# Performance work log

Measured on AMD Instinct MI355X. Metric: run time of the kernel, lower is better.

## Reference

```python
import jax, jax.numpy as jnp
import numpy as np

HIDDEN_DIM = 4096
NUM_EXPERTS = 64
THRESHOLD = 0.8


def setup_inputs() -> dict:
    key = jax.random.key(0)
    kx, kw = jax.random.split(key)
    x = jax.random.normal(kx, (4, 4096, HIDDEN_DIM), dtype=jnp.float32)
    # gate weight init: normal(0, 0.1), bias zeros (as in nn.init calls)
    W = jax.random.normal(kw, (HIDDEN_DIM, NUM_EXPERTS), dtype=jnp.float32) * 0.1
    b = jnp.zeros((NUM_EXPERTS,), dtype=jnp.float32)
    return {"x": x, "W": W, "b": b}


def reference(x, W, b):
    # logits: [B, S, E]
    logits = jnp.einsum('bsh,he->bse', x, W) + b
    probs = jax.nn.softmax(logits, axis=-1)
    # descending sort over experts
    order = jnp.argsort(-probs, axis=-1)                        # [B,S,E] int
    sorted_probs = jnp.take_along_axis(probs, order, axis=-1)   # [B,S,E]
    cum = jnp.cumsum(sorted_probs, axis=-1)
    mask = cum >= THRESHOLD                                     # [B,S,E] bool
    k_values = jnp.argmax(mask.astype(jnp.float32), axis=-1) + 1
    never = ~jnp.any(mask, axis=-1)
    k_values = jnp.where(never, NUM_EXPERTS, k_values)          # [B,S] int
    # Vectorized mask-and-scatter replacing the per-token Python loop.
    # Padded to NUM_EXPERTS (static max_k) for jit compatibility; slots
    # beyond k get expert=-1, prob=0 exactly as the torch fill defaults.
    slot = jnp.arange(NUM_EXPERTS)                              # [E]
    sel = slot[None, None, :] < k_values[..., None]             # [B,S,E]
    selected_experts = jnp.where(sel, order, -1)
    selected_probs = jnp.where(sel, sorted_probs, 0.0)
    return selected_experts, selected_probs, k_values
```

## Files before the change

kernel.cpp:

```cpp
#include <hip/hip_runtime.h>
#include <math.h>

#define HID 4096
#define NEXP 64
#define NTOK 16384
#define PSTR 65

typedef __attribute__((ext_vector_type(8))) short short8;
typedef __attribute__((ext_vector_type(8))) __bf16 bf16x8;
typedef __attribute__((ext_vector_type(4))) float f32x4;

__global__ __launch_bounds__(256) void wfrag_kernel(
    const float* __restrict__ W, short* __restrict__ wfh,
    short* __restrict__ wfl, unsigned int* __restrict__ flag_count) {
  if (blockIdx.x == 0 && threadIdx.x == 0) *flag_count = 0u;
  int gid = blockIdx.x * 256 + threadIdx.x;
  int l  = gid & 63;
  int nt = (gid >> 6) & 3;
  int ks = gid >> 8;
  int e  = nt * 16 + (l & 15);
  int k0 = ks * 32 + (l >> 4) * 8;
  bf16x8 h8, l8;
#pragma unroll
  for (int j = 0; j < 8; ++j) {
    float w = W[(size_t)(k0 + j) * NEXP + e];
    __bf16 h = (__bf16)w;
    h8[j] = h;
    l8[j] = (__bf16)(w - (float)h);
  }
  ((short8*)wfh)[gid] = __builtin_bit_cast(short8, h8);
  ((short8*)wfl)[gid] = __builtin_bit_cast(short8, l8);
}

template <int P>
__device__ __forceinline__ void issue_b(const short8* wh, const short8* wl,
                                        short8 (&rbh)[2][4],
                                        short8 (&rbl)[2][4], int cc) {
#pragma unroll
  for (int nt = 0; nt < 4; ++nt) {
    rbh[P][nt] = wh[cc * 256 + nt * 64];
    rbl[P][nt] = wl[cc * 256 + nt * 64];
  }
}

template <int P>
__device__ __forceinline__ void issue_g(const float* const (&xp)[4][2],
                                        float* wavebase, int cc) {
#pragma unroll
  for (int st = 0; st < 4; ++st)
#pragma unroll
    for (int p = 0; p < 2; ++p)
      __builtin_amdgcn_global_load_lds(xp[st][p] + cc * 32,
                                       wavebase + P * 2048 + st * 512 + p * 256,
                                       16, 0, 0);
}

template <int P>
__device__ __forceinline__ void compute_c(const float* wavebase,
                                          short8 (&rbh)[2][4],
                                          short8 (&rbl)[2][4],
                                          f32x4 (&acc)[4][4], int l) {
  const int lr = l >> 4;
  const int s0 = ((2 * lr) ^ (l & 7)) * 16;
  const char* cb = (const char*)(wavebase + P * 2048);
#pragma unroll
  for (int st = 0; st < 4; ++st) {
    const char* rowbase =
        cb + st * 2048 + ((l >> 3) & 1) * 1024 + (l & 7) * 128;
    float4 lo = *(const float4*)(rowbase + s0);
    float4 hi = *(const float4*)(rowbase + (s0 ^ 16));
    float xv[8] = {lo.x, lo.y, lo.z, lo.w, hi.x, hi.y, hi.z, hi.w};
    bf16x8 ah, al;
#pragma unroll
    for (int j = 0; j < 8; ++j) {
      __bf16 h = (__bf16)xv[j];
      ah[j] = h;
      al[j] = (__bf16)(xv[j] - (float)h);
    }
#pragma unroll
    for (int nt = 0; nt < 4; ++nt) {
      bf16x8 vh = __builtin_bit_cast(bf16x8, rbh[P][nt]);
      bf16x8 vl = __builtin_bit_cast(bf16x8, rbl[P][nt]);
      acc[st][nt] = __builtin_amdgcn_mfma_f32_16x16x32_bf16(ah, vh, acc[st][nt], 0, 0, 0);
      acc[st][nt] = __builtin_amdgcn_mfma_f32_16x16x32_bf16(al, vh, acc[st][nt], 0, 0, 0);
      acc[st][nt] = __builtin_amdgcn_mfma_f32_16x16x32_bf16(ah, vl, acc[st][nt], 0, 0, 0);
      acc[st][nt] = __builtin_amdgcn_mfma_f32_16x16x32_bf16(al, vl, acc[st][nt], 0, 0, 0);
    }
  }
}

#define SB __builtin_amdgcn_sched_barrier(0)
#define WAIT16 asm volatile("s_waitcnt vmcnt(16)" ::: "memory")
#define WAIT0  asm volatile("s_waitcnt vmcnt(0)" ::: "memory")

__global__ __launch_bounds__(512, 2) void gemm_route_kernel(
    const float* __restrict__ x, const short* __restrict__ wfh,
    const short* __restrict__ wfl, const float* __restrict__ b,
    float* __restrict__ out_exp, float* __restrict__ out_prob,
    float* __restrict__ out_k, unsigned int* __restrict__ flag_count,
    int* __restrict__ flag_list) {
  __shared__ float smem[8 * 64 * PSTR];

  const int t = threadIdx.x;
  const int w = t >> 6;
  const int l = t & 63;
  const int lr = l >> 4;
  const int m0 = blockIdx.x * 64;
  const int kq = w * (HID / 8);
  const int start = (blockIdx.x >> 3) & 15;

  float* wavebase = smem + w * 4096;

  const float* xp[4][2];
#pragma unroll
  for (int st = 0; st < 4; ++st)
#pragma unroll
    for (int p = 0; p < 2; ++p) {
      int g = (l & 7) ^ (l >> 3);
      int row = m0 + st * 16 + 8 * p + (l >> 3);
      xp[st][p] = x + (size_t)row * HID + kq + g * 4;
    }

  const short8* wh = (const short8*)wfh + (size_t)(w * 16) * 256 + l;
  const short8* wl = (const short8*)wfl + (size_t)(w * 16) * 256 + l;

  f32x4 acc[4][4];
#pragma unroll
  for (int st = 0; st < 4; ++st)
#pragma unroll
    for (int nt = 0; nt < 4; ++nt) acc[st][nt] = (f32x4){0.f, 0.f, 0.f, 0.f};

  short8 rbh[2][4], rbl[2][4];

  issue_b<0>(wh, wl, rbh, rbl, start);
  SB;
  issue_g<0>(xp, wavebase, start);
  SB;

#pragma unroll 1
  for (int c2 = 0; c2 < 7; ++c2) {
    const int i0 = 2 * c2;
    issue_b<1>(wh, wl, rbh, rbl, (start + i0 + 1) & 15);
    SB;
    issue_g<1>(xp, wavebase, (start + i0 + 1) & 15);
    SB;
    WAIT16;
    SB;
    compute_c<0>(wavebase, rbh, rbl, acc, l);

    issue_b<0>(wh, wl, rbh, rbl, (start + i0 + 2) & 15);
    SB;
    issue_g<0>(xp, wavebase, (start + i0 + 2) & 15);
    SB;
    WAIT16;
    SB;
    compute_c<1>(wavebase, rbh, rbl, acc, l);
  }
  issue_b<1>(wh, wl, rbh, rbl, (start + 15) & 15);
  SB;
  issue_g<1>(xp, wavebase, (start + 15) & 15);
  SB;
  WAIT16;
  SB;
  compute_c<0>(wavebase, rbh, rbl, acc, l);
  WAIT0;
  SB;
  compute_c<1>(wavebase, rbh, rbl, acc, l);

  __syncthreads();
  float* part = smem;
#pragma unroll
  for (int st = 0; st < 4; ++st)
#pragma unroll
    for (int nt = 0; nt < 4; ++nt)
#pragma unroll
      for (int r = 0; r < 4; ++r)
        part[(w * 64 + st * 16 + lr * 4 + r) * PSTR + nt * 16 + (l & 15)] =
            acc[st][nt][r];
  __syncthreads();

  const float bias = b[l];
  for (int it = 0; it < 8; ++it) {
    const int tl = w * 8 + it;
    float a0 = part[(0 * 64 + tl) * PSTR + l];
    float a1 = part[(1 * 64 + tl) * PSTR + l];
    float a2 = part[(2 * 64 + tl) * PSTR + l];
    float a3 = part[(3 * 64 + tl) * PSTR + l];
    float a4 = part[(4 * 64 + tl) * PSTR + l];
    float a5 = part[(5 * 64 + tl) * PSTR + l];
    float a6 = part[(6 * 64 + tl) * PSTR + l];
    float a7 = part[(7 * 64 + tl) * PSTR + l];
    float lgv = ((a0 + a1) + (a2 + a3)) + ((a4 + a5) + (a6 + a7)) + bias;

    float mx = lgv;
#pragma unroll
    for (int off = 32; off; off >>= 1) mx = fmaxf(mx, __shfl_xor(mx, off));
    float ev = expf(lgv - mx);
    float sm = ev;
#pragma unroll
    for (int off = 32; off; off >>= 1) sm += __shfl_xor(sm, off);
    float pr = ev / sm;

    float sp = pr;
    int   si = l;
#pragma unroll
    for (int k = 2; k <= 64; k <<= 1) {
#pragma unroll
      for (int j = k >> 1; j > 0; j >>= 1) {
        float op = __shfl_xor(sp, j);
        int   oi = __shfl_xor(si, j);
        bool cmp  = (sp > op) || (sp == op && si < oi);
        bool keep = (cmp == (((l & k) == 0) == ((l & j) == 0)));
        if (!keep) { sp = op; si = oi; }
      }
    }

    float c = sp;
#pragma unroll
    for (int off = 1; off < 64; off <<= 1) {
      float tp = __shfl_up(c, off);
      if (l >= off) c += tp;
    }

    unsigned long long m = __ballot(c >= 0.8f);
    int kv = (m == 0ULL) ? NEXP : __ffsll(m);

    float spn = __shfl_down(sp, 1);
    bool pairRisk = (l < kv) && (l < 63) && ((sp - spn) < 1e-3f * (sp + spn));
    bool cumRisk  = fabsf(c - 0.8f) < 3e-4f;
    bool flagged  = (__ballot(pairRisk || cumRisk) != 0ULL);

    bool sel = l < kv;
    const int tok = m0 + tl;
    size_t base = (size_t)tok * NEXP;
    out_exp[base + l]  = sel ? (float)si : -1.0f;
    out_prob[base + l] = sel ? sp : 0.0f;
    if (l == 0) {
      out_k[tok] = (float)kv;
      if (flagged) {
        unsigned int idx = atomicAdd(flag_count, 1u);
        flag_list[idx] = tok;
      }
    }
  }
}

__global__ __launch_bounds__(256) void router_repair(
    const float* __restrict__ x, const float* __restrict__ W,
    const float* __restrict__ b, const unsigned int* __restrict__ flag_count,
    const int* __restrict__ flag_list, float* __restrict__ out_exp,
    float* __restrict__ out_prob, float* __restrict__ out_k) {
  __shared__ double part[4][NEXP];
  const int t = threadIdx.x;
  const int e = t & 63;
  const int c = t >> 6;
  const int n = (int)*flag_count;

  for (int i = blockIdx.x; i < n; i += gridDim.x) {
    const int tok = flag_list[i];
    const float* xrow = x + (size_t)tok * HID;
    double s = 0.0;
    const int k0 = c * (HID / 4);
#pragma unroll 8
    for (int k = k0; k < k0 + HID / 4; ++k)
      s = fma((double)xrow[k], (double)W[(size_t)k * NEXP + e], s);
    part[c][e] = s;
    __syncthreads();

    if (t < 64) {
      double lgv = ((part[0][e] + part[1][e]) + part[2][e]) + part[3][e] +
                   (double)b[e];
      double mx = lgv;
#pragma unroll
      for (int off = 32; off; off >>= 1) mx = fmax(mx, __shfl_xor(mx, off));
      double ev = exp(lgv - mx);
      double sm = ev;
#pragma unroll
      for (int off = 32; off; off >>= 1) sm += __shfl_xor(sm, off);
      double p = ev / sm;

      double sp = p;
      int    si = e;
#pragma unroll
      for (int k = 2; k <= 64; k <<= 1) {
#pragma unroll
        for (int j = k >> 1; j > 0; j >>= 1) {
          double op = __shfl_xor(sp, j);
          int    oi = __shfl_xor(si, j);
          bool cmp  = (sp > op) || (sp == op && si < oi);
          bool keep = (cmp == (((e & k) == 0) == ((e & j) == 0)));
          if (!keep) { sp = op; si = oi; }
        }
      }

      double cc = sp;
#pragma unroll
      for (int off = 1; off < 64; off <<= 1) {
        double tp = __shfl_up(cc, off);
        if (e >= off) cc += tp;
      }

      unsigned long long m = __ballot(cc >= 0.8);
      int kv = (m == 0ULL) ? NEXP : __ffsll(m);

      bool sel = e < kv;
      size_t base = (size_t)tok * NEXP;
      out_exp[base + e]  = sel ? (float)si : -1.0f;
      out_prob[base + e] = sel ? (float)sp : 0.0f;
      if (e == 0) out_k[tok] = (float)kv;
    }
    __syncthreads();
  }
}

extern "C" void kernel_launch(void* const* d_in, const int* in_sizes, int n_in,
                              void* d_out, int out_size, void* d_ws,
                              size_t ws_size, hipStream_t stream) {
  const float* x = (const float*)d_in[0];
  const float* W = (const float*)d_in[1];
  const float* b = (const float*)d_in[2];

  float* out_exp  = (float*)d_out;
  float* out_prob = out_exp + (size_t)NTOK * NEXP;
  float* out_k    = out_prob + (size_t)NTOK * NEXP;

  short* wfh = (short*)d_ws;
  short* wfl = (short*)((char*)d_ws + (size_t)512 * 1024);
  unsigned int* flag_count = (unsigned int*)((char*)d_ws + (size_t)1024 * 1024);
  int* flag_list = (int*)((char*)d_ws + (size_t)1024 * 1024 + 256);

  wfrag_kernel<<<128, 256, 0, stream>>>(W, wfh, wfl, flag_count);
  gemm_route_kernel<<<NTOK / 64, 512, 0, stream>>>(
      x, wfh, wfl, b, out_exp, out_prob, out_k, flag_count, flag_list);
  router_repair<<<128, 256, 0, stream>>>(x, W, b, flag_count, flag_list,
                                         out_exp, out_prob, out_k);
}
```

Before: 118.2 us.

## Fuse fp64 repair into GEMM kernel and deepen weight-fragment prefetch pipeline

Drops the separate router_repair launch. Each GEMM block now collects its flagged tokens in shared memory and recomputes them in fp64 in-block after routing, removing the global atomic list and one kernel launch. The K loop is fully unrolled with compile-time chunk steps, and the weight-fragment register buffer goes from 2 to 4 stages so B loads are issued two chunks ahead. The old per-block rotated start chunk is removed. Risks are higher register pressure from the extra buffers, a tail on blocks that have flagged tokens, and loss of the staggering that spread the weight reads across blocks.

```diff
diff --git a/kernel.cpp b/kernel.cpp
--- a/kernel.cpp
+++ b/kernel.cpp
@@ -12,8 +12,7 @@
 
 __global__ __launch_bounds__(256) void wfrag_kernel(
     const float* __restrict__ W, short* __restrict__ wfh,
-    short* __restrict__ wfl, unsigned int* __restrict__ flag_count) {
-  if (blockIdx.x == 0 && threadIdx.x == 0) *flag_count = 0u;
+    short* __restrict__ wfl) {
   int gid = blockIdx.x * 256 + threadIdx.x;
   int l  = gid & 63;
   int nt = (gid >> 6) & 3;
@@ -32,14 +31,19 @@
   ((short8*)wfl)[gid] = __builtin_bit_cast(short8, l8);
 }
 
-template <int P>
+#define SB __builtin_amdgcn_sched_barrier(0)
+#define WAIT24 asm volatile("s_waitcnt vmcnt(24)" ::: "memory")
+#define WAIT16 asm volatile("s_waitcnt vmcnt(16)" ::: "memory")
+#define WAIT0  asm volatile("s_waitcnt vmcnt(0)" ::: "memory")
+
+template <int S>
 __device__ __forceinline__ void issue_b(const short8* wh, const short8* wl,
-                                        short8 (&rbh)[2][4],
-                                        short8 (&rbl)[2][4], int cc) {
+                                        short8 (&rbh)[4][4],
+                                        short8 (&rbl)[4][4], int cc) {
 #pragma unroll
   for (int nt = 0; nt < 4; ++nt) {
-    rbh[P][nt] = wh[cc * 256 + nt * 64];
-    rbl[P][nt] = wl[cc * 256 + nt * 64];
+    rbh[S][nt] = wh[cc * 256 + nt * 64];
+    rbl[S][nt] = wl[cc * 256 + nt * 64];
   }
 }
 
@@ -55,10 +59,10 @@
                                        16, 0, 0);
 }
 
-template <int P>
+template <int P, int S>
 __device__ __forceinline__ void compute_c(const float* wavebase,
-                                          short8 (&rbh)[2][4],
-                                          short8 (&rbl)[2][4],
+                                          short8 (&rbh)[4][4],
+                                          short8 (&rbl)[4][4],
                                           f32x4 (&acc)[4][4], int l) {
   const int lr = l >> 4;
   const int s0 = ((2 * lr) ^ (l & 7)) * 16;
@@ -79,8 +83,8 @@
     }
 #pragma unroll
     for (int nt = 0; nt < 4; ++nt) {
-      bf16x8 vh = __builtin_bit_cast(bf16x8, rbh[P][nt]);
-      bf16x8 vl = __builtin_bit_cast(bf16x8, rbl[P][nt]);
+      bf16x8 vh = __builtin_bit_cast(bf16x8, rbh[S][nt]);
+      bf16x8 vl = __builtin_bit_cast(bf16x8, rbl[S][nt]);
       acc[st][nt] = __builtin_amdgcn_mfma_f32_16x16x32_bf16(ah, vh, acc[st][nt], 0, 0, 0);
       acc[st][nt] = __builtin_amdgcn_mfma_f32_16x16x32_bf16(al, vh, acc[st][nt], 0, 0, 0);
       acc[st][nt] = __builtin_amdgcn_mfma_f32_16x16x32_bf16(ah, vl, acc[st][nt], 0, 0, 0);
@@ -89,17 +93,33 @@
   }
 }
 
-#define SB __builtin_amdgcn_sched_barrier(0)
-#define WAIT16 asm volatile("s_waitcnt vmcnt(16)" ::: "memory")
-#define WAIT0  asm volatile("s_waitcnt vmcnt(0)" ::: "memory")
+template <int N>
+__device__ __forceinline__ void chunk_step(const float* const (&xp)[4][2],
+                                           float* wavebase, const short8* wh,
+                                           const short8* wl,
+                                           short8 (&rbh)[4][4],
+                                           short8 (&rbl)[4][4],
+                                           f32x4 (&acc)[4][4], int l) {
+  if constexpr (N + 1 < 16) issue_g<(N + 1) & 1>(xp, wavebase, N + 1);
+  SB;
+  if constexpr (N + 2 < 16) issue_b<(N + 2) & 3>(wh, wl, rbh, rbl, N + 2);
+  SB;
+  if constexpr (N <= 13) { WAIT24; }
+  else if constexpr (N == 14) { WAIT16; }
+  else { WAIT0; }
+  SB;
+  compute_c<N & 1, N & 3>(wavebase, rbh, rbl, acc, l);
+  SB;
+}
 
 __global__ __launch_bounds__(512, 2) void gemm_route_kernel(
-    const float* __restrict__ x, const short* __restrict__ wfh,
-    const short* __restrict__ wfl, const float* __restrict__ b,
-    float* __restrict__ out_exp, float* __restrict__ out_prob,
-    float* __restrict__ out_k, unsigned int* __restrict__ flag_count,
-    int* __restrict__ flag_list) {
+    const float* __restrict__ x, const float* __restrict__ W,
+    const short* __restrict__ wfh, const short* __restrict__ wfl,
+    const float* __restrict__ b, float* __restrict__ out_exp,
+    float* __restrict__ out_prob, float* __restrict__ out_k) {
   __shared__ float smem[8 * 64 * PSTR];
+  __shared__ int s_cnt;
+  __shared__ int s_toks[64];
 
   const int t = threadIdx.x;
   const int w = t >> 6;
@@ -107,7 +127,8 @@
   const int lr = l >> 4;
   const int m0 = blockIdx.x * 64;
   const int kq = w * (HID / 8);
-  const int start = (blockIdx.x >> 3) & 15;
+
+  if (t == 0) s_cnt = 0;
 
   float* wavebase = smem + w * 4096;
 
@@ -130,42 +151,31 @@
 #pragma unroll
     for (int nt = 0; nt < 4; ++nt) acc[st][nt] = (f32x4){0.f, 0.f, 0.f, 0.f};
 
-  short8 rbh[2][4], rbl[2][4];
-
-  issue_b<0>(wh, wl, rbh, rbl, start);
-  SB;
-  issue_g<0>(xp, wavebase, start);
-  SB;
-
-#pragma unroll 1
-  for (int c2 = 0; c2 < 7; ++c2) {
-    const int i0 = 2 * c2;
-    issue_b<1>(wh, wl, rbh, rbl, (start + i0 + 1) & 15);
-    SB;
-    issue_g<1>(xp, wavebase, (start + i0 + 1) & 15);
-    SB;
-    WAIT16;
-    SB;
-    compute_c<0>(wavebase, rbh, rbl, acc, l);
-
-    issue_b<0>(wh, wl, rbh, rbl, (start + i0 + 2) & 15);
-    SB;
-    issue_g<0>(xp, wavebase, (start + i0 + 2) & 15);
-    SB;
-    WAIT16;
-    SB;
-    compute_c<1>(wavebase, rbh, rbl, acc, l);
-  }
-  issue_b<1>(wh, wl, rbh, rbl, (start + 15) & 15);
-  SB;
-  issue_g<1>(xp, wavebase, (start + 15) & 15);
-  SB;
-  WAIT16;
-  SB;
-  compute_c<0>(wavebase, rbh, rbl, acc, l);
-  WAIT0;
-  SB;
-  compute_c<1>(wavebase, rbh, rbl, acc, l);
+  short8 rbh[4][4], rbl[4][4];
+
+  issue_b<0>(wh, wl, rbh, rbl, 0);
+  SB;
+  issue_g<0>(xp, wavebase, 0);
+  SB;
+  issue_b<1>(wh, wl, rbh, rbl, 1);
+  SB;
+
+  chunk_step<0>(xp, wavebase, wh, wl, rbh, rbl, acc, l);
+  chunk_step<1>(xp, wavebase, wh, wl, rbh, rbl, acc, l);
+  chunk_step<2>(xp, wavebase, wh, wl, rbh, rbl, acc, l);
+  chunk_step<3>(xp, wavebase, wh, wl, rbh, rbl, acc, l);
+  chunk_step<4>(xp, wavebase, wh, wl, rbh, rbl, acc, l);
+  chunk_step<5>(xp, wavebase, wh, wl, rbh, rbl, acc, l);
+  chunk_step<6>(xp, wavebase, wh, wl, rbh, rbl, acc, l);
+  chunk_step<7>(xp, wavebase, wh, wl, rbh, rbl, acc, l);
+  chunk_step<8>(xp, wavebase, wh, wl, rbh, rbl, acc, l);
+  chunk_step<9>(xp, wavebase, wh, wl, rbh, rbl, acc, l);
+  chunk_step<10>(xp, wavebase, wh, wl, rbh, rbl, acc, l);
+  chunk_step<11>(xp, wavebase, wh, wl, rbh, rbl, acc, l);
+  chunk_step<12>(xp, wavebase, wh, wl, rbh, rbl, acc, l);
+  chunk_step<13>(xp, wavebase, wh, wl, rbh, rbl, acc, l);
+  chunk_step<14>(xp, wavebase, wh, wl, rbh, rbl, acc, l);
+  chunk_step<15>(xp, wavebase, wh, wl, rbh, rbl, acc, l);
 
   __syncthreads();
   float* part = smem;
@@ -238,38 +248,39 @@
     if (l == 0) {
       out_k[tok] = (float)kv;
       if (flagged) {
-        unsigned int idx = atomicAdd(flag_count, 1u);
-        flag_list[idx] = tok;
+        int idx = atomicAdd(&s_cnt, 1);
+        if (idx < 64) s_toks[idx] = tl;
       }
     }
   }
-}
-
-__global__ __launch_bounds__(256) void router_repair(
-    const float* __restrict__ x, const float* __restrict__ W,
-    const float* __restrict__ b, const unsigned int* __restrict__ flag_count,
-    const int* __restrict__ flag_list, float* __restrict__ out_exp,
-    float* __restrict__ out_prob, float* __restrict__ out_k) {
-  __shared__ double part[4][NEXP];
-  const int t = threadIdx.x;
-  const int e = t & 63;
-  const int c = t >> 6;
-  const int n = (int)*flag_count;
-
-  for (int i = blockIdx.x; i < n; i += gridDim.x) {
-    const int tok = flag_list[i];
-    const float* xrow = x + (size_t)tok * HID;
-    double s = 0.0;
-    const int k0 = c * (HID / 4);
+
+  __syncthreads();
+  int cnt = s_cnt;
+  if (cnt > 64) cnt = 64;
+  double* dpart = (double*)smem;
+  const int g = w >> 2;
+  const int q = w & 3;
+
+  for (int i = 0; i < cnt; i += 2) {
+    const int which = i + g;
+    const bool active = which < cnt;
+    int tok = 0;
+    if (active) {
+      tok = m0 + s_toks[which];
+      const float* xr = x + (size_t)tok * HID;
+      double s = 0.0;
+      const int k0 = q * (HID / 4);
 #pragma unroll 8
-    for (int k = k0; k < k0 + HID / 4; ++k)
-      s = fma((double)xrow[k], (double)W[(size_t)k * NEXP + e], s);
-    part[c][e] = s;
+      for (int k = k0; k < k0 + HID / 4; ++k)
+        s = fma((double)xr[k], (double)W[(size_t)k * NEXP + l], s);
+      dpart[(g * 4 + q) * 64 + l] = s;
+    }
     __syncthreads();
-
-    if (t < 64) {
-      double lgv = ((part[0][e] + part[1][e]) + part[2][e]) + part[3][e] +
-                   (double)b[e];
+    if (active && q == 0) {
+      double lgv = ((dpart[(g * 4 + 0) * 64 + l] + dpart[(g * 4 + 1) * 64 + l]) +
+                    dpart[(g * 4 + 2) * 64 + l]) +
+                   dpart[(g * 4 + 3) * 64 + l] + (double)b[l];
+
       double mx = lgv;
 #pragma unroll
       for (int off = 32; off; off >>= 1) mx = fmax(mx, __shfl_xor(mx, off));
@@ -280,7 +291,7 @@
       double p = ev / sm;
 
       double sp = p;
-      int    si = e;
+      int    si = l;
 #pragma unroll
       for (int k = 2; k <= 64; k <<= 1) {
 #pragma unroll
@@ -288,7 +299,7 @@
           double op = __shfl_xor(sp, j);
           int    oi = __shfl_xor(si, j);
           bool cmp  = (sp > op) || (sp == op && si < oi);
-          bool keep = (cmp == (((e & k) == 0) == ((e & j) == 0)));
+          bool keep = (cmp == (((l & k) == 0) == ((l & j) == 0)));
           if (!keep) { sp = op; si = oi; }
         }
       }
@@ -297,17 +308,17 @@
 #pragma unroll
       for (int off = 1; off < 64; off <<= 1) {
         double tp = __shfl_up(cc, off);
-        if (e >= off) cc += tp;
+        if (l >= off) cc += tp;
       }
 
       unsigned long long m = __ballot(cc >= 0.8);
       int kv = (m == 0ULL) ? NEXP : __ffsll(m);
 
-      bool sel = e < kv;
+      bool sel = l < kv;
       size_t base = (size_t)tok * NEXP;
-      out_exp[base + e]  = sel ? (float)si : -1.0f;
-      out_prob[base + e] = sel ? (float)sp : 0.0f;
-      if (e == 0) out_k[tok] = (float)kv;
+      out_exp[base + l]  = sel ? (float)si : -1.0f;
+      out_prob[base + l] = sel ? (float)sp : 0.0f;
+      if (l == 0) out_k[tok] = (float)kv;
     }
     __syncthreads();
   }
@@ -326,12 +337,8 @@
 
   short* wfh = (short*)d_ws;
   short* wfl = (short*)((char*)d_ws + (size_t)512 * 1024);
-  unsigned int* flag_count = (unsigned int*)((char*)d_ws + (size_t)1024 * 1024);
-  int* flag_list = (int*)((char*)d_ws + (size_t)1024 * 1024 + 256);
-
-  wfrag_kernel<<<128, 256, 0, stream>>>(W, wfh, wfl, flag_count);
+
+  wfrag_kernel<<<128, 256, 0, stream>>>(W, wfh, wfl);
   gemm_route_kernel<<<NTOK / 64, 512, 0, stream>>>(
-      x, wfh, wfl, b, out_exp, out_prob, out_k, flag_count, flag_list);
-  router_repair<<<128, 256, 0, stream>>>(x, W, b, flag_count, flag_list,
-                                         out_exp, out_prob, out_k);
-}
+      x, W, wfh, wfl, b, out_exp, out_prob, out_k);
+}
```

Measured after the change: 136.1 us. 1.15x slower.
